# Optimization experiments

Measured on AMD Instinct MI355X. Metric: run time of the kernel, lower is better.

## Reference

```python
import jax, jax.numpy as jnp
import numpy as np
from jax import lax

NPOINT = 1024
RADIUS = 0.4
NSAMPLE = 32
BN_EPS = 1e-5


def _square_distance(src, dst):
    # src [B,S,3], dst [B,N,3] -> [B,S,N]
    d = -2.0 * jnp.einsum('bsc,bnc->bsn', src, dst)
    d = d + jnp.sum(src ** 2, -1)[:, :, None]
    d = d + jnp.sum(dst ** 2, -1)[:, None, :]
    return d


def _farthest_point_sample(xyz, npoint):
    # xyz [B,N,3] -> int32 indices [B,npoint]
    B, N, _ = xyz.shape
    # deterministic start at index 0 (torch uses randint; math is otherwise identical)
    init_far = jnp.zeros((B,), dtype=jnp.int32)
    init_dist = jnp.full((B, N), 1e10, dtype=xyz.dtype)

    def step(carry, _):
        distance, farthest = carry
        centroid = jnp.take_along_axis(xyz, farthest[:, None, None], axis=1)  # [B,1,3]
        dist = jnp.sum((xyz - centroid) ** 2, -1)  # [B,N]
        distance = jnp.minimum(distance, dist)
        new_far = jnp.argmax(distance, axis=-1).astype(jnp.int32)
        return (distance, new_far), farthest

    (_, _), cents = lax.scan(step, (init_dist, init_far), None, length=npoint)
    return cents.T  # [B, npoint]


def _query_ball_point(radius, nsample, xyz, new_xyz):
    # xyz [B,N,3], new_xyz [B,S,3] -> idx [B,S,nsample]
    B, N, _ = xyz.shape
    sqr = _square_distance(new_xyz, xyz)  # [B,S,N]
    ar = jnp.arange(N, dtype=jnp.int32)
    gi = jnp.where(sqr > radius * radius, N, ar[None, None, :])
    gi = jnp.sort(gi, axis=-1)[:, :, :nsample]
    first = gi[:, :, :1]
    return jnp.where(gi == N, first, gi)


def setup_inputs() -> dict:
    key = jax.random.key(0)
    ks = jax.random.split(key, 8)
    B, N = 16, 4096
    inp = {
        'xyz': jax.random.normal(ks[0], (B, 3, N), jnp.float32),
        'points': jax.random.normal(ks[1], (B, 6, N), jnp.float32),
    }
    dims = [(64, 9), (64, 64), (128, 64)]
    for i, (o, c) in enumerate(dims):
        inp[f'w{i}'] = jax.random.normal(ks[2 + i], (o, c), jnp.float32) * 0.05
        inp[f'b{i}'] = jnp.zeros((o,), jnp.float32)
        inp[f'g{i}'] = jnp.ones((o,), jnp.float32)
        inp[f'beta{i}'] = jnp.zeros((o,), jnp.float32)
    return inp


def reference(xyz, points, w0, b0, g0, beta0, w1, b1, g1, beta1, w2, b2, g2, beta2):
    # xyz [B,3,N], points [B,6,N]
    xyz_t = jnp.transpose(xyz, (0, 2, 1))      # [B,N,3]
    pts_t = jnp.transpose(points, (0, 2, 1))   # [B,N,6]
    B, N, _ = xyz_t.shape
    S, ns = NPOINT, NSAMPLE

    fps_idx = _farthest_point_sample(xyz_t, S)                 # [B,S]
    new_xyz = jnp.take_along_axis(xyz_t, fps_idx[:, :, None], axis=1)  # [B,S,3]
    idx = _query_ball_point(RADIUS, ns, xyz_t, new_xyz)        # [B,S,ns]
    flat = idx.reshape(B, S * ns, 1)
    g_xyz = jnp.take_along_axis(xyz_t, flat, axis=1).reshape(B, S, ns, 3)
    g_xyz = g_xyz - new_xyz[:, :, None, :]                     # grouped_xyz_norm
    g_pts = jnp.take_along_axis(pts_t, flat, axis=1).reshape(B, S, ns, -1)
    feat = jnp.concatenate([g_xyz, g_pts], axis=-1)            # [B,S,ns,9]

    # shared MLP: 1x1 conv + BatchNorm (training-mode batch stats) + ReLU
    for w, b, g, be in ((w0, b0, g0, beta0), (w1, b1, g1, beta1), (w2, b2, g2, beta2)):
        h = jnp.einsum('bsnc,oc->bsno', feat, w) + b
        mu = jnp.mean(h, axis=(0, 1, 2))
        var = jnp.var(h, axis=(0, 1, 2))
        feat = jax.nn.relu((h - mu) * lax.rsqrt(var + BN_EPS) * g + be)

    new_points = jnp.max(feat, axis=2)                         # max over nsample -> [B,S,Cout]
    return (jnp.transpose(new_xyz, (0, 2, 1)), jnp.transpose(new_points, (0, 2, 1)))
```

## Files before the change

kernel.cpp:

```cpp
#include <hip/hip_runtime.h>
#include <hip/hip_bf16.h>
#include <stdint.h>

#define NB 16
#define NP 4096
#define NSP 1024
#define KNN 32
#define PTOT (NB*NSP*KNN)
#define NTILES (PTOT/16)

typedef __attribute__((ext_vector_type(8))) short short8;
typedef __attribute__((ext_vector_type(4))) float f32x4;

__device__ __forceinline__ float fadd_(float a,float b){return __fadd_rn(a,b);}
__device__ __forceinline__ float fmul_(float a,float b){return __fmul_rn(a,b);}
__device__ __forceinline__ float fsub_(float a,float b){return __fsub_rn(a,b);}

__device__ __forceinline__ float bf2f(unsigned short u){
    unsigned int x = ((unsigned int)u) << 16; float f; __builtin_memcpy(&f,&x,4); return f;
}
__device__ __forceinline__ unsigned short f2bf(float f){
    unsigned int x; __builtin_memcpy(&x,&f,4);
    x = x + 0x7fffu + ((x>>16)&1u);
    return (unsigned short)(x>>16);
}

template<int CTRL>
__device__ __forceinline__ unsigned long long dpp_max_step(unsigned long long v){
    unsigned int lo = (unsigned int)v, hi = (unsigned int)(v>>32);
    unsigned int lod = (unsigned int)__builtin_amdgcn_update_dpp(0, (int)lo, CTRL, 0xF, 0xF, true);
    unsigned int hid = (unsigned int)__builtin_amdgcn_update_dpp(0, (int)hi, CTRL, 0xF, 0xF, true);
    unsigned long long o = ((unsigned long long)hid<<32) | lod;
    return (o > v) ? o : v;
}

__global__ __launch_bounds__(256,1) void fps_kernel(const float* __restrict__ xyz,
    int* __restrict__ fps_idx)
{
    const int b = blockIdx.x, tid = threadIdx.x;
    const int lane = tid & 63, wv = tid >> 6;
    const float* xb = xyz + (size_t)b*3*NP;
    __shared__ float4 sp[NP];
    __shared__ unsigned long long slots[2][4];
    __shared__ int farr[NSP];
    float px[16],py[16],pz[16],pd[16];
    const int base = tid*16;
#pragma unroll
    for (int j=0;j<16;j+=4){
        float4 vx = *(const float4*)(xb + base + j);
        float4 vy = *(const float4*)(xb + NP + base + j);
        float4 vz = *(const float4*)(xb + 2*NP + base + j);
        px[j]=vx.x; px[j+1]=vx.y; px[j+2]=vx.z; px[j+3]=vx.w;
        py[j]=vy.x; py[j+1]=vy.y; py[j+2]=vy.z; py[j+3]=vy.w;
        pz[j]=vz.x; pz[j+1]=vz.y; pz[j+2]=vz.z; pz[j+3]=vz.w;
        sp[base+j+0] = make_float4(vx.x,vy.x,vz.x,0.f);
        sp[base+j+1] = make_float4(vx.y,vy.y,vz.y,0.f);
        sp[base+j+2] = make_float4(vx.z,vy.z,vz.z,0.f);
        sp[base+j+3] = make_float4(vx.w,vy.w,vz.w,0.f);
        pd[j]=1e10f; pd[j+1]=1e10f; pd[j+2]=1e10f; pd[j+3]=1e10f;
    }
    __syncthreads();
    int far = 0;
    float cx, cy, cz;
    { float4 c0 = sp[0]; cx=c0.x; cy=c0.y; cz=c0.z; }
    for (int s=0;s<NSP;s++){
        if (tid==0) farr[s] = far;
        float bd=-1.0f; int bi=0;
#pragma unroll
        for (int j=0;j<16;j++){
            float dx=fsub_(px[j],cx), dy=fsub_(py[j],cy), dz=fsub_(pz[j],cz);
            float d = fadd_(fadd_(fmul_(dx,dx),fmul_(dy,dy)),fmul_(dz,dz));
            float nd = fminf(pd[j], d); pd[j]=nd;
            if (nd > bd){ bd=nd; bi=base+j; }
        }
        unsigned int hb; __builtin_memcpy(&hb,&bd,4);
        unsigned long long best = ((unsigned long long)hb<<32) | (unsigned int)(NP-1-bi);
        best = dpp_max_step<0x111>(best);
        best = dpp_max_step<0x112>(best);
        best = dpp_max_step<0x114>(best);
        best = dpp_max_step<0x118>(best);
        best = dpp_max_step<0x142>(best);
        best = dpp_max_step<0x143>(best);
        if (lane==63) slots[s&1][wv] = best;
        __syncthreads();
        {
            const unsigned long long* sl = slots[s&1];
            unsigned long long a0 = sl[0], a1 = sl[1], a2 = sl[2], a3 = sl[3];
            unsigned long long m0 = a0>a1?a0:a1, m1 = a2>a3?a2:a3;
            unsigned long long m  = m0>m1?m0:m1;
            far = NP-1-(int)(m & 0xFFFFFFFFu);
        }
        float4 c = sp[far]; cx=c.x; cy=c.y; cz=c.z;
    }
    __syncthreads();
    for (int i=tid;i<NSP;i+=256) fps_idx[b*NSP+i] = farr[i];
}

__global__ void centroid_kernel(const float* __restrict__ xyz, const int* __restrict__ fps_idx,
    float* __restrict__ new_xyz, float* __restrict__ out0)
{
    int t = blockIdx.x*256 + threadIdx.x;
    if (t >= NB*NSP) return;
    int b = t>>10, s = t&1023;
    int id = fps_idx[t];
    const float* xb = xyz + (size_t)b*3*NP;
    float x=xb[id], y=xb[NP+id], z=xb[2*NP+id];
    float* nz = new_xyz + (size_t)t*3;
    nz[0]=x; nz[1]=y; nz[2]=z;
    out0[(size_t)b*3*NSP + s]         = x;
    out0[(size_t)b*3*NSP + NSP + s]   = y;
    out0[(size_t)b*3*NSP + 2*NSP + s] = z;
}

__global__ __launch_bounds__(256,1) void ball_gather_kernel(const float* __restrict__ xyz,
    const float* __restrict__ pts, const float* __restrict__ new_xyz,
    unsigned short* __restrict__ feat)
{
    const int lane = threadIdx.x & 63, wv = threadIdx.x >> 6;
    const int center = blockIdx.x*4 + wv;
    const int b = center >> 10;
    const float* xb = xyz + (size_t)b*3*NP;
    const float* pb = pts + (size_t)b*6*NP;
    const float* nz = new_xyz + (size_t)center*3;
    const float cx=nz[0], cy=nz[1], cz=nz[2];
    const float src2 = fadd_(fadd_(fmul_(cx,cx),fmul_(cy,cy)),fmul_(cz,cz));
    const float R2 = (float)(0.4*0.4);
    __shared__ int slots[4][32];
    int total = 0;
    for (int c0=0;c0<NP;c0+=64){
        const int i = c0 + lane;
        float x=xb[i], y=xb[NP+i], z=xb[2*NP+i];
        float dot  = fadd_(fadd_(fmul_(cx,x),fmul_(cy,y)),fmul_(cz,z));
        float dst2 = fadd_(fadd_(fmul_(x,x),fmul_(y,y)),fmul_(z,z));
        float d = fadd_(fadd_(fmul_(-2.0f,dot), src2), dst2);
        bool pred = !(d > R2);
        unsigned long long m = __ballot(pred);
        int pos = total + (int)__popcll(m & ((1ull<<lane)-1ull));
        if (pred && pos < 32) slots[wv][pos] = i;
        total += (int)__popcll(m);
        if (total >= 32) break;
    }
    const int nvalid = total < 32 ? total : 32;
    __syncthreads();
    const int n = lane & 31;
    const int idx = slots[wv][ (n < nvalid) ? n : 0 ];
    unsigned short* fr = feat + (size_t)center*KNN*32 + (size_t)n*32;
    if (lane < 32){
        float gx = fsub_(xb[idx], cx), gy = fsub_(xb[NP+idx], cy), gz = fsub_(xb[2*NP+idx], cz);
        float p0=pb[idx], p1=pb[NP+idx], p2=pb[2*NP+idx], p3=pb[3*NP+idx], p4=pb[4*NP+idx];
        short8 v;
        v[0]=(short)f2bf(gx); v[1]=(short)f2bf(gy); v[2]=(short)f2bf(gz);
        v[3]=(short)f2bf(p0); v[4]=(short)f2bf(p1); v[5]=(short)f2bf(p2);
        v[6]=(short)f2bf(p3); v[7]=(short)f2bf(p4);
        *(short8*)fr = v;
    } else {
        float p5 = pb[5*NP+idx];
        short8 v = (short8){0,0,0,0,0,0,0,0};
        v[0]=(short)f2bf(p5);
        *(short8*)(fr+8)  = v;
        short8 z8 = (short8){0,0,0,0,0,0,0,0};
        *(short8*)(fr+16) = z8;
        *(short8*)(fr+24) = z8;
    }
}

template<int KT,int OT,bool NORM_IN,bool STORE_H>
__global__ __launch_bounds__(256,1) void conv_kernel(const unsigned short* __restrict__ in,
    const unsigned short* __restrict__ wp, const float* __restrict__ bias,
    const float* __restrict__ nAB, unsigned short* __restrict__ h_out,
    double* __restrict__ stats)
{
    constexpr int K = KT*32, O = OT*16;
    const int lane = threadIdx.x & 63, wv = threadIdx.x >> 6;
    const int col = lane & 15, quad = lane >> 4;
    short8 bf[OT][KT];
#pragma unroll
    for (int t=0;t<OT;t++)
#pragma unroll
        for (int kt=0;kt<KT;kt++)
            bf[t][kt] = *(const short8*)(wp + (size_t)(t*16+col)*K + kt*32 + quad*8);
    float brow[OT];
#pragma unroll
    for (int t=0;t<OT;t++) brow[t] = bias[t*16+col];
    float nA[KT*8], nB[KT*8];
    if constexpr (NORM_IN){
#pragma unroll
        for (int kt=0;kt<KT;kt++)
#pragma unroll
            for (int j=0;j<8;j++){
                int c = kt*32+quad*8+j;
                nA[kt*8+j]=nAB[c]; nB[kt*8+j]=nAB[128+c];
            }
    }
    float ssum[OT], ssq[OT];
#pragma unroll
    for (int t=0;t<OT;t++){ ssum[t]=0.f; ssq[t]=0.f; }
    const int gw = blockIdx.x*4 + wv, nw = gridDim.x*4;
    for (int tile=gw; tile<NTILES; tile+=nw){
        const int row0 = tile*16;
        short8 af[KT];
#pragma unroll
        for (int kt=0;kt<KT;kt++){
            af[kt] = *(const short8*)(in + (size_t)(row0+col)*K + kt*32 + quad*8);
            if constexpr (NORM_IN){
#pragma unroll
                for (int j=0;j<8;j++){
                    float x = bf2f((unsigned short)af[kt][j]);
                    x = fmaxf(x*nA[kt*8+j]+nB[kt*8+j], 0.f);
                    af[kt][j] = (short)f2bf(x);
                }
            }
        }
        f32x4 acc[OT];
#pragma unroll
        for (int t=0;t<OT;t++) acc[t] = (f32x4){0.f,0.f,0.f,0.f};
#pragma unroll
        for (int kt=0;kt<KT;kt++)
#pragma unroll
            for (int t=0;t<OT;t++)
                acc[t] = __builtin_amdgcn_mfma_f32_16x16x32_bf16(af[kt], bf[t][kt], acc[t], 0,0,0);
#pragma unroll
        for (int t=0;t<OT;t++){
#pragma unroll
            for (int r=0;r<4;r++){
                float h = acc[t][r] + brow[t];
                if constexpr (STORE_H)
                    h_out[(size_t)(row0 + quad*4 + r)*O + t*16 + col] = f2bf(h);
                ssum[t] += h; ssq[t] = fmaf(h,h,ssq[t]);
            }
        }
    }
    __shared__ float bsum[128], bssq[128];
    for (int i=threadIdx.x;i<128;i+=256){ bsum[i]=0.f; bssq[i]=0.f; }
    __syncthreads();
#pragma unroll
    for (int t=0;t<OT;t++){
        float v = ssum[t]; v += __shfl_xor(v,16,64); v += __shfl_xor(v,32,64);
        float q = ssq[t];  q += __shfl_xor(q,16,64); q += __shfl_xor(q,32,64);
        if (quad==0){ atomicAdd(&bsum[t*16+col], v); atomicAdd(&bssq[t*16+col], q); }
    }
    __syncthreads();
    if ((int)threadIdx.x < O){
        const int slot = blockIdx.x & 7;
        atomicAdd(&stats[(size_t)(slot*2+0)*128 + threadIdx.x], (double)bsum[threadIdx.x]);
        atomicAdd(&stats[(size_t)(slot*2+1)*128 + threadIdx.x], (double)bssq[threadIdx.x]);
    }
}

__global__ void finalize_kernel(const double* __restrict__ stats, const float* __restrict__ g,
    const float* __restrict__ beta, float* __restrict__ AB, int O)
{
    int o = threadIdx.x;
    if (o >= O) return;
    double s=0.0, q=0.0;
#pragma unroll
    for (int slot=0;slot<8;slot++){
        s += stats[(size_t)(slot*2+0)*128+o];
        q += stats[(size_t)(slot*2+1)*128+o];
    }
    const double cnt = (double)PTOT;
    float mean = (float)(s/cnt);
    float var  = (float)(q/cnt - (s/cnt)*(s/cnt));
    float inv  = rsqrtf(var + 1e-5f);
    float A = g[o]*inv;
    AB[o] = A; AB[128+o] = beta[o] - mean*A;
}

__global__ __launch_bounds__(256,1) void conv_final_kernel(const unsigned short* __restrict__ in,
    const unsigned short* __restrict__ wp, const float* __restrict__ bias,
    const float* __restrict__ nABin, const float* __restrict__ nABout,
    float* __restrict__ out1)
{
    constexpr int KT=2, OT=8, K=64;
    const int lane = threadIdx.x & 63, wv = threadIdx.x >> 6;
    const int col = lane & 15, quad = lane >> 4;
    short8 bf[OT][KT];
#pragma unroll
    for (int t=0;t<OT;t++)
#pragma unroll
        for (int kt=0;kt<KT;kt++)
            bf[t][kt] = *(const short8*)(wp + (size_t)(t*16+col)*K + kt*32 + quad*8);
    float brow[OT], oA[OT], oB[OT];
#pragma unroll
    for (int t=0;t<OT;t++){
        brow[t] = bias[t*16+col];
        oA[t] = nABout[t*16+col];
        oB[t] = nABout[128+t*16+col];
    }
    float nA[16], nB[16];
#pragma unroll
    for (int kt=0;kt<2;kt++)
#pragma unroll
        for (int j=0;j<8;j++){
            int c = kt*32+quad*8+j;
            nA[kt*8+j]=nABin[c]; nB[kt*8+j]=nABin[128+c];
        }
    const int gw = blockIdx.x*4 + wv, nw = gridDim.x*4;
    for (int grp=gw; grp<NB*NSP; grp+=nw){
        float vmax[OT];
#pragma unroll
        for (int t=0;t<OT;t++) vmax[t]=0.f;
#pragma unroll
        for (int mt=0; mt<2; mt++){
            const int row0 = grp*32 + mt*16;
            short8 af[KT];
#pragma unroll
            for (int kt=0;kt<2;kt++){
                af[kt] = *(const short8*)(in + (size_t)(row0+col)*K + kt*32 + quad*8);
#pragma unroll
                for (int j=0;j<8;j++){
                    float x = bf2f((unsigned short)af[kt][j]);
                    x = fmaxf(x*nA[kt*8+j]+nB[kt*8+j], 0.f);
                    af[kt][j] = (short)f2bf(x);
                }
            }
            f32x4 acc[OT];
#pragma unroll
            for (int t=0;t<OT;t++) acc[t] = (f32x4){0.f,0.f,0.f,0.f};
#pragma unroll
            for (int kt=0;kt<2;kt++)
#pragma unroll
                for (int t=0;t<OT;t++)
                    acc[t] = __builtin_amdgcn_mfma_f32_16x16x32_bf16(af[kt], bf[t][kt], acc[t], 0,0,0);
#pragma unroll
            for (int t=0;t<OT;t++){
#pragma unroll
                for (int r=0;r<4;r++){
                    float h = acc[t][r] + brow[t];
                    float x = fmaxf(h*oA[t]+oB[t], 0.f);
                    vmax[t] = fmaxf(vmax[t], x);
                }
            }
        }
#pragma unroll
        for (int t=0;t<OT;t++){
            float v = vmax[t];
            v = fmaxf(v, __shfl_xor(v,16,64));
            v = fmaxf(v, __shfl_xor(v,32,64));
            if (quad==0){
                int o = t*16+col, bb = grp>>10, ss = grp&1023;
                out1[((size_t)bb*128+o)*NSP + ss] = v;
            }
        }
    }
}

__global__ void prep_kernel(const float* __restrict__ w0, const float* __restrict__ w1,
    const float* __restrict__ w2, unsigned short* __restrict__ wp0,
    unsigned short* __restrict__ wp1, unsigned short* __restrict__ wp2)
{
    int t = blockIdx.x*256 + threadIdx.x;
    if (t < 64*32){ int o=t>>5, c=t&31; wp0[t] = (c<9) ? f2bf(w0[o*9+c]) : (unsigned short)0; }
    if (t < 64*64)  wp1[t] = f2bf(w1[t]);
    if (t < 128*64) wp2[t] = f2bf(w2[t]);
}

extern "C" void kernel_launch(void* const* d_in, const int* in_sizes, int n_in,
                              void* d_out, int out_size, void* d_ws, size_t ws_size,
                              hipStream_t stream)
{
    (void)in_sizes; (void)n_in; (void)out_size; (void)ws_size;
    const float* xyz = (const float*)d_in[0];
    const float* pts = (const float*)d_in[1];
    const float* w0  = (const float*)d_in[2];
    const float* b0  = (const float*)d_in[3];
    const float* g0  = (const float*)d_in[4];
    const float* be0 = (const float*)d_in[5];
    const float* w1  = (const float*)d_in[6];
    const float* b1  = (const float*)d_in[7];
    const float* g1  = (const float*)d_in[8];
    const float* be1 = (const float*)d_in[9];
    const float* w2  = (const float*)d_in[10];
    const float* b2  = (const float*)d_in[11];
    const float* g2  = (const float*)d_in[12];
    const float* be2 = (const float*)d_in[13];

    char* ws = (char*)d_ws;
    size_t off = 0;
    auto alloc = [&](size_t sz)->char*{ char* p = ws + off; off = (off + sz + 255) & ~(size_t)255; return p; };
    int*            fps_idx = (int*)           alloc((size_t)NB*NSP*4);
    float*          new_xyz = (float*)         alloc((size_t)NB*NSP*3*4);
    unsigned short* wp0     = (unsigned short*)alloc(64*32*2);
    unsigned short* wp1     = (unsigned short*)alloc(64*64*2);
    unsigned short* wp2     = (unsigned short*)alloc(128*64*2);
    double*         stats   = (double*)        alloc((size_t)3*8*2*128*8);
    float*          AB0     = (float*)         alloc(256*4);
    float*          AB1     = (float*)         alloc(256*4);
    float*          AB2     = (float*)         alloc(256*4);
    unsigned short* feat    = (unsigned short*)alloc((size_t)PTOT*32*2);
    unsigned short* h0      = (unsigned short*)alloc((size_t)PTOT*64*2);
    unsigned short* h1      = (unsigned short*)alloc((size_t)PTOT*64*2);

    float* out0 = (float*)d_out;
    float* out1 = out0 + (size_t)NB*3*NSP;

    hipMemsetAsync(stats, 0, (size_t)3*8*2*128*8, stream);
    prep_kernel<<<32,256,0,stream>>>(w0,w1,w2,wp0,wp1,wp2);
    fps_kernel<<<NB,256,0,stream>>>(xyz, fps_idx);
    centroid_kernel<<<(NB*NSP+255)/256,256,0,stream>>>(xyz, fps_idx, new_xyz, out0);
    ball_gather_kernel<<<NB*NSP/4,256,0,stream>>>(xyz, pts, new_xyz, feat);
    conv_kernel<1,4,false,true><<<1024,256,0,stream>>>(feat, wp0, b0, nullptr, h0, stats);
    finalize_kernel<<<1,128,0,stream>>>(stats, g0, be0, AB0, 64);
    conv_kernel<2,4,true,true><<<1024,256,0,stream>>>(h0, wp1, b1, AB0, h1, stats + 2048);
    finalize_kernel<<<1,128,0,stream>>>(stats + 2048, g1, be1, AB1, 64);
    conv_kernel<2,8,true,false><<<1024,256,0,stream>>>(h1, wp2, b2, AB1, nullptr, stats + 4096);
    finalize_kernel<<<1,128,0,stream>>>(stats + 4096, g2, be2, AB2, 128);
    conv_final_kernel<<<2048,256,0,stream>>>(h1, wp2, b2, AB1, AB2, out1);
}
```

Baseline: 873.5 us.

## Fuse centroid and BN-finalize kernels into neighbors; tree-reduce FPS argmax

The centroid kernel is removed. Ball-gather now reads fps indices directly, loads the centroid coordinates itself and writes out0. The three finalize kernels are folded into the prologues of the following conv kernels, and each block recomputes the BN scale and shift from the double stats into shared memory. FPS now writes its indices straight to global memory instead of staging them in shared memory, and replaces the serial per-thread argmax with packed 64-bit keys and a pairwise tree max to shorten the dependency chain. The aim is fewer launches and lower FPS latency, at the cost of redundant per-block stats reduction.

```diff
diff --git a/kernel.cpp b/kernel.cpp
--- a/kernel.cpp
+++ b/kernel.cpp
@@ -42,8 +42,8 @@
     const float* xb = xyz + (size_t)b*3*NP;
     __shared__ float4 sp[NP];
     __shared__ unsigned long long slots[2][4];
-    __shared__ int farr[NSP];
     float px[16],py[16],pz[16],pd[16];
+    unsigned int lowc[16];
     const int base = tid*16;
 #pragma unroll
     for (int j=0;j<16;j+=4){
@@ -58,23 +58,33 @@
         sp[base+j+2] = make_float4(vx.z,vy.z,vz.z,0.f);
         sp[base+j+3] = make_float4(vx.w,vy.w,vz.w,0.f);
         pd[j]=1e10f; pd[j+1]=1e10f; pd[j+2]=1e10f; pd[j+3]=1e10f;
+        lowc[j]   = (unsigned int)(NP-1-(base+j));
+        lowc[j+1] = (unsigned int)(NP-1-(base+j+1));
+        lowc[j+2] = (unsigned int)(NP-1-(base+j+2));
+        lowc[j+3] = (unsigned int)(NP-1-(base+j+3));
     }
     __syncthreads();
     int far = 0;
     float cx, cy, cz;
     { float4 c0 = sp[0]; cx=c0.x; cy=c0.y; cz=c0.z; }
     for (int s=0;s<NSP;s++){
-        if (tid==0) farr[s] = far;
-        float bd=-1.0f; int bi=0;
+        if (tid==0) fps_idx[b*NSP+s] = far;
 #pragma unroll
         for (int j=0;j<16;j++){
             float dx=fsub_(px[j],cx), dy=fsub_(py[j],cy), dz=fsub_(pz[j],cz);
             float d = fadd_(fadd_(fmul_(dx,dx),fmul_(dy,dy)),fmul_(dz,dz));
-            float nd = fminf(pd[j], d); pd[j]=nd;
-            if (nd > bd){ bd=nd; bi=base+j; }
-        }
-        unsigned int hb; __builtin_memcpy(&hb,&bd,4);
-        unsigned long long best = ((unsigned long long)hb<<32) | (unsigned int)(NP-1-bi);
+            pd[j] = fminf(pd[j], d);
+        }
+        unsigned long long k[16];
+#pragma unroll
+        for (int j=0;j<16;j++)
+            k[j] = ((unsigned long long)__float_as_uint(pd[j])<<32) | lowc[j];
+#pragma unroll
+        for (int st=1; st<16; st<<=1)
+#pragma unroll
+            for (int j=0;j<16;j+=2*st)
+                k[j] = (k[j+st] > k[j]) ? k[j+st] : k[j];
+        unsigned long long best = k[0];
         best = dpp_max_step<0x111>(best);
         best = dpp_max_step<0x112>(best);
         best = dpp_max_step<0x114>(best);
@@ -92,37 +102,24 @@
         }
         float4 c = sp[far]; cx=c.x; cy=c.y; cz=c.z;
     }
-    __syncthreads();
-    for (int i=tid;i<NSP;i+=256) fps_idx[b*NSP+i] = farr[i];
-}
-
-__global__ void centroid_kernel(const float* __restrict__ xyz, const int* __restrict__ fps_idx,
-    float* __restrict__ new_xyz, float* __restrict__ out0)
-{
-    int t = blockIdx.x*256 + threadIdx.x;
-    if (t >= NB*NSP) return;
-    int b = t>>10, s = t&1023;
-    int id = fps_idx[t];
-    const float* xb = xyz + (size_t)b*3*NP;
-    float x=xb[id], y=xb[NP+id], z=xb[2*NP+id];
-    float* nz = new_xyz + (size_t)t*3;
-    nz[0]=x; nz[1]=y; nz[2]=z;
-    out0[(size_t)b*3*NSP + s]         = x;
-    out0[(size_t)b*3*NSP + NSP + s]   = y;
-    out0[(size_t)b*3*NSP + 2*NSP + s] = z;
 }
 
 __global__ __launch_bounds__(256,1) void ball_gather_kernel(const float* __restrict__ xyz,
-    const float* __restrict__ pts, const float* __restrict__ new_xyz,
-    unsigned short* __restrict__ feat)
+    const float* __restrict__ pts, const int* __restrict__ fps_idx,
+    unsigned short* __restrict__ feat, float* __restrict__ out0)
 {
     const int lane = threadIdx.x & 63, wv = threadIdx.x >> 6;
     const int center = blockIdx.x*4 + wv;
-    const int b = center >> 10;
+    const int b = center >> 10, s = center & 1023;
     const float* xb = xyz + (size_t)b*3*NP;
     const float* pb = pts + (size_t)b*6*NP;
-    const float* nz = new_xyz + (size_t)center*3;
-    const float cx=nz[0], cy=nz[1], cz=nz[2];
+    const int id = fps_idx[center];
+    const float cx=xb[id], cy=xb[NP+id], cz=xb[2*NP+id];
+    if (lane==0){
+        out0[(size_t)b*3*NSP + s]         = cx;
+        out0[(size_t)b*3*NSP + NSP + s]   = cy;
+        out0[(size_t)b*3*NSP + 2*NSP + s] = cz;
+    }
     const float src2 = fadd_(fadd_(fmul_(cx,cx),fmul_(cy,cy)),fmul_(cz,cz));
     const float R2 = (float)(0.4*0.4);
     __shared__ int slots[4][32];
@@ -164,15 +161,41 @@
     }
 }
 
+__device__ __forceinline__ void compute_AB(const double* __restrict__ stats,
+    const float* __restrict__ g, const float* __restrict__ beta,
+    float* sA, float* sB, int K, int o)
+{
+    if (o >= 0 && o < K){
+        double s=0.0, q=0.0;
+#pragma unroll
+        for (int slot=0;slot<8;slot++){
+            s += stats[(size_t)(slot*2+0)*128+o];
+            q += stats[(size_t)(slot*2+1)*128+o];
+        }
+        const double cnt = (double)PTOT;
+        float mean = (float)(s/cnt);
+        float var  = (float)(q/cnt - (s/cnt)*(s/cnt));
+        float inv  = rsqrtf(var + 1e-5f);
+        float A = g[o]*inv;
+        sA[o] = A; sB[o] = beta[o] - mean*A;
+    }
+}
+
 template<int KT,int OT,bool NORM_IN,bool STORE_H>
 __global__ __launch_bounds__(256,1) void conv_kernel(const unsigned short* __restrict__ in,
     const unsigned short* __restrict__ wp, const float* __restrict__ bias,
-    const float* __restrict__ nAB, unsigned short* __restrict__ h_out,
-    double* __restrict__ stats)
+    const double* __restrict__ stats_in, const float* __restrict__ g_in,
+    const float* __restrict__ beta_in, unsigned short* __restrict__ h_out,
+    double* __restrict__ stats_out)
 {
     constexpr int K = KT*32, O = OT*16;
     const int lane = threadIdx.x & 63, wv = threadIdx.x >> 6;
     const int col = lane & 15, quad = lane >> 4;
+    __shared__ float sA[128], sB[128];
+    if constexpr (NORM_IN){
+        compute_AB(stats_in, g_in, beta_in, sA, sB, K, (int)threadIdx.x);
+        __syncthreads();
+    }
     short8 bf[OT][KT];
 #pragma unroll
     for (int t=0;t<OT;t++)
@@ -189,7 +212,7 @@
 #pragma unroll
             for (int j=0;j<8;j++){
                 int c = kt*32+quad*8+j;
-                nA[kt*8+j]=nAB[c]; nB[kt*8+j]=nAB[128+c];
+                nA[kt*8+j]=sA[c]; nB[kt*8+j]=sB[c];
             }
     }
     float ssum[OT], ssq[OT];
@@ -242,38 +265,24 @@
     __syncthreads();
     if ((int)threadIdx.x < O){
         const int slot = blockIdx.x & 7;
-        atomicAdd(&stats[(size_t)(slot*2+0)*128 + threadIdx.x], (double)bsum[threadIdx.x]);
-        atomicAdd(&stats[(size_t)(slot*2+1)*128 + threadIdx.x], (double)bssq[threadIdx.x]);
-    }
-}
-
-__global__ void finalize_kernel(const double* __restrict__ stats, const float* __restrict__ g,
-    const float* __restrict__ beta, float* __restrict__ AB, int O)
-{
-    int o = threadIdx.x;
-    if (o >= O) return;
-    double s=0.0, q=0.0;
-#pragma unroll
-    for (int slot=0;slot<8;slot++){
-        s += stats[(size_t)(slot*2+0)*128+o];
-        q += stats[(size_t)(slot*2+1)*128+o];
-    }
-    const double cnt = (double)PTOT;
-    float mean = (float)(s/cnt);
-    float var  = (float)(q/cnt - (s/cnt)*(s/cnt));
-    float inv  = rsqrtf(var + 1e-5f);
-    float A = g[o]*inv;
-    AB[o] = A; AB[128+o] = beta[o] - mean*A;
+        atomicAdd(&stats_out[(size_t)(slot*2+0)*128 + threadIdx.x], (double)bsum[threadIdx.x]);
+        atomicAdd(&stats_out[(size_t)(slot*2+1)*128 + threadIdx.x], (double)bssq[threadIdx.x]);
+    }
 }
 
 __global__ __launch_bounds__(256,1) void conv_final_kernel(const unsigned short* __restrict__ in,
     const unsigned short* __restrict__ wp, const float* __restrict__ bias,
-    const float* __restrict__ nABin, const float* __restrict__ nABout,
+    const double* __restrict__ stats1, const float* __restrict__ g1, const float* __restrict__ be1,
+    const double* __restrict__ stats2, const float* __restrict__ g2, const float* __restrict__ be2,
     float* __restrict__ out1)
 {
     constexpr int KT=2, OT=8, K=64;
     const int lane = threadIdx.x & 63, wv = threadIdx.x >> 6;
     const int col = lane & 15, quad = lane >> 4;
+    __shared__ float sA1[128], sB1[128], sA2[128], sB2[128];
+    compute_AB(stats1, g1, be1, sA1, sB1, 64,  (int)threadIdx.x);
+    compute_AB(stats2, g2, be2, sA2, sB2, 128, (int)threadIdx.x - 128);
+    __syncthreads();
     short8 bf[OT][KT];
 #pragma unroll
     for (int t=0;t<OT;t++)
@@ -284,8 +293,8 @@
 #pragma unroll
     for (int t=0;t<OT;t++){
         brow[t] = bias[t*16+col];
-        oA[t] = nABout[t*16+col];
-        oB[t] = nABout[128+t*16+col];
+        oA[t] = sA2[t*16+col];
+        oB[t] = sB2[t*16+col];
     }
     float nA[16], nB[16];
 #pragma unroll
@@ -293,7 +302,7 @@
 #pragma unroll
         for (int j=0;j<8;j++){
             int c = kt*32+quad*8+j;
-            nA[kt*8+j]=nABin[c]; nB[kt*8+j]=nABin[128+c];
+            nA[kt*8+j]=sA1[c]; nB[kt*8+j]=sB1[c];
         }
     const int gw = blockIdx.x*4 + wv, nw = gridDim.x*4;
     for (int grp=gw; grp<NB*NSP; grp+=nw){
@@ -379,31 +388,24 @@
     size_t off = 0;
     auto alloc = [&](size_t sz)->char*{ char* p = ws + off; off = (off + sz + 255) & ~(size_t)255; return p; };
     int*            fps_idx = (int*)           alloc((size_t)NB*NSP*4);
-    float*          new_xyz = (float*)         alloc((size_t)NB*NSP*3*4);
     unsigned short* wp0     = (unsigned short*)alloc(64*32*2);
     unsigned short* wp1     = (unsigned short*)alloc(64*64*2);
     unsigned short* wp2     = (unsigned short*)alloc(128*64*2);
     double*         stats   = (double*)        alloc((size_t)3*8*2*128*8);
-    float*          AB0     = (float*)         alloc(256*4);
-    float*          AB1     = (float*)         alloc(256*4);
-    float*          AB2     = (float*)         alloc(256*4);
     unsigned short* feat    = (unsigned short*)alloc((size_t)PTOT*32*2);
     unsigned short* h0      = (unsigned short*)alloc((size_t)PTOT*64*2);
     unsigned short* h1      = (unsigned short*)alloc((size_t)PTOT*64*2);
 
     float* out0 = (float*)d_out;
     float* out1 = out0 + (size_t)NB*3*NSP;
+    double* stats0 = stats, *stats1 = stats + 2048, *stats2 = stats + 4096;
 
     hipMemsetAsync(stats, 0, (size_t)3*8*2*128*8, stream);
     prep_kernel<<<32,256,0,stream>>>(w0,w1,w2,wp0,wp1,wp2);
     fps_kernel<<<NB,256,0,stream>>>(xyz, fps_idx);
-    centroid_kernel<<<(NB*NSP+255)/256,256,0,stream>>>(xyz, fps_idx, new_xyz, out0);
-    ball_gather_kernel<<<NB*NSP/4,256,0,stream>>>(xyz, pts, new_xyz, feat);
-    conv_kernel<1,4,false,true><<<1024,256,0,stream>>>(feat, wp0, b0, nullptr, h0, stats);
-    finalize_kernel<<<1,128,0,stream>>>(stats, g0, be0, AB0, 64);
-    conv_kernel<2,4,true,true><<<1024,256,0,stream>>>(h0, wp1, b1, AB0, h1, stats + 2048);
-    finalize_kernel<<<1,128,0,stream>>>(stats + 2048, g1, be1, AB1, 64);
-    conv_kernel<2,8,true,false><<<1024,256,0,stream>>>(h1, wp2, b2, AB1, nullptr, stats + 4096);
-    finalize_kernel<<<1,128,0,stream>>>(stats + 4096, g2, be2, AB2, 128);
-    conv_final_kernel<<<2048,256,0,stream>>>(h1, wp2, b2, AB1, AB2, out1);
-}
+    ball_gather_kernel<<<NB*NSP/4,256,0,stream>>>(xyz, pts, fps_idx, feat, out0);
+    conv_kernel<1,4,false,true><<<1024,256,0,stream>>>(feat, wp0, b0, nullptr,nullptr,nullptr, h0, stats0);
+    conv_kernel<2,4,true,true><<<1024,256,0,stream>>>(h0, wp1, b1, stats0, g0, be0, h1, stats1);
+    conv_kernel<2,8,true,false><<<1024,256,0,stream>>>(h1, wp2, b2, stats1, g1, be1, nullptr, stats2);
+    conv_final_kernel<<<2048,256,0,stream>>>(h1, wp2, b2, stats1, g1, be1, stats2, g2, be2, out1);
+}
```

Measured after the change: 878.8 us. About the same (+0.6%).
